# Kernel tuning notes

Hardware: AMD Instinct MI355X
Metric: run time of the kernel (lower is better)

The kernel has to match this reference:

```python
import jax, jax.numpy as jnp
import numpy as np

WH = WW = 8          # window height/width
N_WIN = WH * WW      # tokens per window = 64
DIM = 256
NUM_HEADS = 8
CPB_HIDDEN = 512


def _rel_index():
    # Swin relative position index, shape (N, N), values in [0, (2Wh-1)*(2Ww-1))
    coords = np.stack(np.meshgrid(np.arange(WH), np.arange(WW), indexing='ij'))  # (2,Wh,Ww)
    flat = coords.reshape(2, -1)
    rel = (flat[:, :, None] - flat[:, None, :]).transpose(1, 2, 0)  # (N,N,2)
    rel[..., 0] += WH - 1
    rel[..., 1] += WW - 1
    rel[..., 0] *= 2 * WW - 1
    return rel.sum(-1).astype(np.int32)


def _coords_table():
    # normalized log-spaced continuous relative coordinates, shape (2Wh-1, 2Ww-1, 2)
    h = np.arange(-(WH - 1), WH, dtype=np.float32)
    w = np.arange(-(WW - 1), WW, dtype=np.float32)
    t = np.stack(np.meshgrid(h, w, indexing='ij'), axis=-1)
    t[..., 0] /= WH - 1
    t[..., 1] /= WW - 1
    t *= 8.0
    return (np.sign(t) * np.log2(np.abs(t) + 1.0) / np.log2(8.0)).astype(np.float32)


def setup_inputs() -> dict:
    key = jax.random.key(0)
    ks = jax.random.split(key, 6)
    B_ = 8192  # num_windows * batch
    x = jax.random.normal(ks[0], (B_, N_WIN, DIM), dtype=jnp.float32)
    qkv_weight = jax.random.normal(ks[1], (3 * DIM, DIM), dtype=jnp.float32) * 0.02
    q_bias = jnp.zeros((DIM,), dtype=jnp.float32)
    v_bias = jnp.zeros((DIM,), dtype=jnp.float32)
    logit_scale = jnp.log(10.0) * jnp.ones((NUM_HEADS, 1, 1), dtype=jnp.float32)
    cpb_w1 = jax.random.normal(ks[2], (CPB_HIDDEN, 2), dtype=jnp.float32) * 0.02
    cpb_b1 = jnp.zeros((CPB_HIDDEN,), dtype=jnp.float32)
    cpb_w2 = jax.random.normal(ks[3], (NUM_HEADS, CPB_HIDDEN), dtype=jnp.float32) * 0.02
    proj_w = jax.random.normal(ks[4], (DIM, DIM), dtype=jnp.float32) * 0.02
    proj_b = jnp.zeros((DIM,), dtype=jnp.float32)
    return {
        'x': x, 'qkv_weight': qkv_weight, 'q_bias': q_bias, 'v_bias': v_bias,
        'logit_scale': logit_scale, 'cpb_w1': cpb_w1, 'cpb_b1': cpb_b1,
        'cpb_w2': cpb_w2, 'proj_w': proj_w, 'proj_b': proj_b,
    }


def reference(x, qkv_weight, q_bias, v_bias, logit_scale, cpb_w1, cpb_b1, cpb_w2, proj_w, proj_b):
    B_, N, C = x.shape
    H = NUM_HEADS
    d = C // H
    # qkv projection: k-bias is fixed zero (Swin-V2 convention)
    qkv_b = jnp.concatenate([q_bias, jnp.zeros_like(v_bias), v_bias])
    qkv = x @ qkv_weight.T + qkv_b                       # (B_, N, 3C)
    qkv = qkv.reshape(B_, N, 3, H, d).transpose(2, 0, 3, 1, 4)  # (3, B_, H, N, d)
    q, k, v = qkv[0], qkv[1], qkv[2]
    # cosine attention (F.normalize with eps=1e-12)
    qn = q / jnp.maximum(jnp.linalg.norm(q, axis=-1, keepdims=True), 1e-12)
    kn = k / jnp.maximum(jnp.linalg.norm(k, axis=-1, keepdims=True), 1e-12)
    attn = jnp.einsum('bhnd,bhmd->bhnm', qn, kn)
    scale = jnp.exp(jnp.minimum(logit_scale, jnp.log(100.0)))  # clamp max = log(1/0.01)
    attn = attn * scale                                   # broadcasts (H,1,1)
    # continuous relative position bias via tiny MLP
    table = jnp.asarray(_coords_table())                  # (2Wh-1, 2Ww-1, 2)
    bias_table = jnp.maximum(table @ cpb_w1.T + cpb_b1, 0.0) @ cpb_w2.T  # (.., H)
    bias_table = bias_table.reshape(-1, H)
    idx = jnp.asarray(_rel_index().reshape(-1))
    bias = bias_table[idx].reshape(N, N, H).transpose(2, 0, 1)  # (H, N, N)
    attn = attn + 16.0 * jax.nn.sigmoid(bias)[None]
    attn = jax.nn.softmax(attn, axis=-1)
    out = jnp.einsum('bhnm,bhmd->bhnd', attn, v)          # (B_, H, N, d)
    out = out.transpose(0, 2, 1, 3).reshape(B_, N, C)
    return out @ proj_w.T + proj_b
```

## Files before the change

kernel.cpp:

```cpp
#include <hip/hip_runtime.h>
#include <hip/hip_fp16.h>

typedef _Float16 f16;
typedef _Float16 f16x8 __attribute__((ext_vector_type(8)));
typedef _Float16 f16x4 __attribute__((ext_vector_type(4)));
typedef float f32x4 __attribute__((ext_vector_type(4)));

#define L2E 1.4426950408889634f

#define WQ_OFF   0
#define PW_OFF   393216
#define QB_OFF   524288
#define SC_OFF   527360
#define TBL_OFF  527616
#define BB_OFF   535040


__global__ void prep0(const float* __restrict__ qw, const float* __restrict__ prw,
                      const float* __restrict__ qbias, const float* __restrict__ vbias,
                      const float* __restrict__ ls, char* __restrict__ ws) {
    int t = blockIdx.x * 256 + threadIdx.x;
    f16* wq = (f16*)(ws + WQ_OFF);
    f16* pw = (f16*)(ws + PW_OFF);
    if (t < 196608) wq[t] = (f16)qw[t];
    else            pw[t - 196608] = (f16)prw[t - 196608];
    if (t < 768) {
        float b = t < 256 ? qbias[t] : (t < 512 ? 0.f : vbias[t - 512]);
        ((float*)(ws + QB_OFF))[t] = b;
    }
    if (t < 8) ((float*)(ws + SC_OFF))[t] = expf(fminf(ls[t], 4.6051701859880914f));
}

__device__ __forceinline__ float norm_coord(int u) {
    float v = (float)(u - 7) * (8.0f / 7.0f);
    float s = (v > 0.f) ? 1.f : ((v < 0.f) ? -1.f : 0.f);
    return s * log2f(fabsf(v) + 1.f) * (1.f / 3.f);
}

__global__ void prep1(const float* __restrict__ w1, const float* __restrict__ b1,
                      const float* __restrict__ w2, char* __restrict__ ws) {
    int t = blockIdx.x * 256 + threadIdx.x;
    if (t >= 1800) return;
    int p = t >> 3, h = t & 7;
    float ta = norm_coord(p / 15);
    float tb = norm_coord(p % 15);
    float acc = 0.f;
    for (int j = 0; j < 512; ++j) {
        float hv = fmaf(w1[2 * j], ta, fmaf(w1[2 * j + 1], tb, b1[j]));
        acc = fmaf(fmaxf(hv, 0.f), w2[h * 512 + j], acc);
    }
    ((float*)(ws + TBL_OFF))[p * 8 + h] = acc;
}

__global__ void prep2(char* __restrict__ ws) {
    int t = blockIdx.x * 256 + threadIdx.x;
    int h = t >> 12, i = (t >> 6) & 63, j = t & 63;
    int ri = ((i >> 3) - (j >> 3) + 7) * 15 + ((i & 7) - (j & 7) + 7);
    float bv = ((const float*)(ws + TBL_OFF))[ri * 8 + h];
    float sg = 1.f / (1.f + expf(-bv));
    float sch = ((const float*)(ws + SC_OFF))[h];
    float val = (16.f * sg - sch - 16.f) * L2E + 14.0f;
    int mi = i >> 4, g = (i >> 2) & 3, r = i & 3;
    int nj = j >> 4, c = j & 15;
    int off = h * 4096 + mi * 1024 + nj * 256 + c * 16 + g * 4 + r;
    ((float*)(ws + BB_OFF))[off] = val;
}

#define SWZ(row) (((row) & 7) << 4)
#define LGKM0() asm volatile("s_waitcnt lgkmcnt(0)" ::: "memory")

__global__ __launch_bounds__(512, 2)
void swin_fused(const float* __restrict__ x, const f16* __restrict__ wq,
                const f16* __restrict__ pw, const float* __restrict__ qb,
                const float* __restrict__ sc, const float* __restrict__ bb2,
                const float* __restrict__ pb, float* __restrict__ out) {
    extern __shared__ char lds[];
    const int tid = threadIdx.x;
    const int lane = tid & 63;
    const int w = tid >> 6;
    const int g = lane >> 4;
    const int c = lane & 15;
    const int win = blockIdx.x;
    char* scr = lds + 32768 + w * 5120;

    const float* xw = x + (size_t)win * 16384;
    #pragma unroll
    for (int it = 0; it < 8; ++it) {
        int e4 = tid + it * 512;
        float4 v = ((const float4*)xw)[e4];
        int eidx = e4 * 4;
        int row = eidx >> 8, col = eidx & 255;
        f16x4 h4 = {(f16)v.x, (f16)v.y, (f16)v.z, (f16)v.w};
        int off = ((row << 9) + (col << 1)) ^ SWZ(row);
        *(f16x4*)(lds + off) = h4;
    }
    __syncthreads();

    f16x8 vf[2][2];
    {
        f32x4 acc[2][4] = {};
        for (int kk = 0; kk < 8; ++kk) {
            int kb = kk * 32 + g * 8;
            f16x8 a[4];
            #pragma unroll
            for (int mi = 0; mi < 4; ++mi) {
                int row = mi * 16 + c;
                int off = ((row << 9) + (kb << 1)) ^ SWZ(row);
                a[mi] = *(const f16x8*)(lds + off);
            }
            #pragma unroll
            for (int t = 0; t < 2; ++t) {
                f16x8 b = *(const f16x8*)(wq + (size_t)(512 + w * 32 + t * 16 + c) * 256 + kb);
                #pragma unroll
                for (int mi = 0; mi < 4; ++mi)
                    acc[t][mi] = __builtin_amdgcn_mfma_f32_16x16x32_f16(a[mi], b, acc[t][mi], 0, 0, 0);
            }
        }
        #pragma unroll
        for (int t = 0; t < 2; ++t) {
            float bias = qb[512 + w * 32 + t * 16 + c];
            #pragma unroll
            for (int mi = 0; mi < 4; ++mi) {
                f16x4 h;
                #pragma unroll
                for (int r = 0; r < 4; ++r) h[r] = (f16)(acc[t][mi][r] + bias);
                int off = (t * 16 + c) * 144 + (mi * 16 + g * 4) * 2;
                *(f16x4*)(scr + off) = h;
            }
        }
    }
    LGKM0();
    #pragma unroll
    for (int dt = 0; dt < 2; ++dt)
        #pragma unroll
        for (int kt = 0; kt < 2; ++kt)
            vf[dt][kt] = *(const f16x8*)(scr + (dt * 16 + c) * 144 + kt * 64 + g * 16);
    LGKM0();

    f16x8 qf[4], kf[4];
    {
        f32x4 aq[2][4] = {};
        for (int kk = 0; kk < 8; ++kk) {
            int kb = kk * 32 + g * 8;
            f16x8 a[4];
            #pragma unroll
            for (int mi = 0; mi < 4; ++mi) {
                int row = mi * 16 + c;
                int off = ((row << 9) + (kb << 1)) ^ SWZ(row);
                a[mi] = *(const f16x8*)(lds + off);
            }
            #pragma unroll
            for (int t = 0; t < 2; ++t) {
                f16x8 bq = *(const f16x8*)(wq + (size_t)(w * 32 + t * 16 + c) * 256 + kb);
                #pragma unroll
                for (int mi = 0; mi < 4; ++mi)
                    aq[t][mi] = __builtin_amdgcn_mfma_f32_16x16x32_f16(a[mi], bq, aq[t][mi], 0, 0, 0);
            }
        }
        #pragma unroll
        for (int t = 0; t < 2; ++t) {
            float bias = qb[w * 32 + t * 16 + c];
            #pragma unroll
            for (int mi = 0; mi < 4; ++mi)
                #pragma unroll
                for (int r = 0; r < 4; ++r) aq[t][mi][r] += bias;
        }
        f32x4 rq[4];
        #pragma unroll
        for (int mi = 0; mi < 4; ++mi) {
            #pragma unroll
            for (int r = 0; r < 4; ++r) {
                float pq = aq[0][mi][r] * aq[0][mi][r] + aq[1][mi][r] * aq[1][mi][r];
                pq += __shfl_xor(pq, 1); pq += __shfl_xor(pq, 2);
                pq += __shfl_xor(pq, 4); pq += __shfl_xor(pq, 8);
                rq[mi][r] = __builtin_amdgcn_rsqf(fmaxf(pq, 1e-24f));
            }
        }
        #pragma unroll
        for (int t = 0; t < 2; ++t)
            #pragma unroll
            for (int mi = 0; mi < 4; ++mi)
                #pragma unroll
                for (int r = 0; r < 4; ++r) {
                    int off = (mi * 16 + g * 4 + r) * 80 + (t * 16 + c) * 2;
                    *(f16*)(scr + off) = (f16)(aq[t][mi][r] * rq[mi][r]);
                }
        LGKM0();
        #pragma unroll
        for (int mi = 0; mi < 4; ++mi)
            qf[mi] = *(const f16x8*)(scr + (mi * 16 + c) * 80 + g * 16);
        LGKM0();
    }
    {
        f32x4 ak[2][4] = {};
        for (int kk = 0; kk < 8; ++kk) {
            int kb = kk * 32 + g * 8;
            f16x8 a[4];
            #pragma unroll
            for (int mi = 0; mi < 4; ++mi) {
                int row = mi * 16 + c;
                int off = ((row << 9) + (kb << 1)) ^ SWZ(row);
                a[mi] = *(const f16x8*)(lds + off);
            }
            #pragma unroll
            for (int t = 0; t < 2; ++t) {
                f16x8 bk = *(const f16x8*)(wq + (size_t)(256 + w * 32 + t * 16 + c) * 256 + kb);
                #pragma unroll
                for (int mi = 0; mi < 4; ++mi)
                    ak[t][mi] = __builtin_amdgcn_mfma_f32_16x16x32_f16(a[mi], bk, ak[t][mi], 0, 0, 0);
            }
        }
        f32x4 rk[4];
        #pragma unroll
        for (int mi = 0; mi < 4; ++mi) {
            #pragma unroll
            for (int r = 0; r < 4; ++r) {
                float pk = ak[0][mi][r] * ak[0][mi][r] + ak[1][mi][r] * ak[1][mi][r];
                pk += __shfl_xor(pk, 1); pk += __shfl_xor(pk, 2);
                pk += __shfl_xor(pk, 4); pk += __shfl_xor(pk, 8);
                rk[mi][r] = __builtin_amdgcn_rsqf(fmaxf(pk, 1e-24f));
            }
        }
        #pragma unroll
        for (int t = 0; t < 2; ++t)
            #pragma unroll
            for (int mi = 0; mi < 4; ++mi)
                #pragma unroll
                for (int r = 0; r < 4; ++r) {
                    int off = (mi * 16 + g * 4 + r) * 80 + (t * 16 + c) * 2;
                    *(f16*)(scr + off) = (f16)(ak[t][mi][r] * rk[mi][r]);
                }
        LGKM0();
        #pragma unroll
        for (int nj = 0; nj < 4; ++nj)
            kf[nj] = *(const f16x8*)(scr + (nj * 16 + c) * 80 + g * 16);
        LGKM0();
    }

    const float scl2e = sc[w] * L2E;
    const float* bbw = bb2 + w * 4096;
    f32x4 o[4][2] = {};
    f32x4 rs[4] = {};
    #pragma unroll
    for (int nj = 0; nj < 4; ++nj) {
        #pragma unroll
        for (int mi = 0; mi < 4; ++mi) {
            f32x4 z = {};
            f32x4 s = __builtin_amdgcn_mfma_f32_16x16x32_f16(qf[mi], kf[nj], z, 0, 0, 0);
            f32x4 bb4 = *(const f32x4*)(bbw + mi * 1024 + nj * 256 + c * 16 + g * 4);
            #pragma unroll
            for (int r = 0; r < 4; ++r) {
                float e = exp2f(fmaf(s[r], scl2e, bb4[r]));
                rs[mi][r] += e;
                int off = (mi * 16 + g * 4 + r) * 80 + (((nj & 1) * 16 + c) << 1);
                *(f16*)(scr + off) = (f16)e;
            }
        }
        if (nj == 1 || nj == 3) {
            const int kt = nj >> 1;
            LGKM0();
            f16x8 pa[4];
            #pragma unroll
            for (int mo = 0; mo < 4; ++mo)
                pa[mo] = *(const f16x8*)(scr + (mo * 16 + c) * 80 + g * 16);
            LGKM0();
            #pragma unroll
            for (int mo = 0; mo < 4; ++mo)
                #pragma unroll
                for (int dt = 0; dt < 2; ++dt)
                    o[mo][dt] = __builtin_amdgcn_mfma_f32_16x16x32_f16(pa[mo], vf[dt][kt], o[mo][dt], 0, 0, 0);
        }
    }
    f32x4 rinv[4];
    #pragma unroll
    for (int mi = 0; mi < 4; ++mi)
        #pragma unroll
        for (int r = 0; r < 4; ++r) {
            float t = rs[mi][r];
            t += __shfl_xor(t, 1); t += __shfl_xor(t, 2);
            t += __shfl_xor(t, 4); t += __shfl_xor(t, 8);
            rinv[mi][r] = __builtin_amdgcn_rcpf(t);
        }

    __syncthreads();
    #pragma unroll
    for (int mi = 0; mi < 4; ++mi)
        #pragma unroll
        for (int dt = 0; dt < 2; ++dt)
            #pragma unroll
            for (int r = 0; r < 4; ++r) {
                int row = mi * 16 + g * 4 + r;
                int col = w * 32 + dt * 16 + c;
                int off = ((row << 9) + (col << 1)) ^ SWZ(row);
                *(f16*)(lds + off) = (f16)(o[mi][dt][r] * rinv[mi][r]);
            }
    __syncthreads();

    f32x4 pacc[2][4] = {};
    for (int kk = 0; kk < 8; ++kk) {
        int kb = kk * 32 + g * 8;
        f16x8 a[4];
        #pragma unroll
        for (int mi = 0; mi < 4; ++mi) {
            int row = mi * 16 + c;
            int off = ((row << 9) + (kb << 1)) ^ SWZ(row);
            a[mi] = *(const f16x8*)(lds + off);
        }
        #pragma unroll
        for (int nt = 0; nt < 2; ++nt) {
            f16x8 b = *(const f16x8*)(pw + (size_t)(w * 32 + nt * 16 + c) * 256 + kb);
            #pragma unroll
            for (int mi = 0; mi < 4; ++mi)
                pacc[nt][mi] = __builtin_amdgcn_mfma_f32_16x16x32_f16(a[mi], b, pacc[nt][mi], 0, 0, 0);
        }
    }
    __syncthreads();

    #pragma unroll
    for (int nt = 0; nt < 2; ++nt) {
        float pbias = pb[w * 32 + nt * 16 + c];
        #pragma unroll
        for (int mi = 0; mi < 4; ++mi)
            #pragma unroll
            for (int r = 0; r < 4; ++r) {
                int row = mi * 16 + g * 4 + r;
                int col = w * 32 + nt * 16 + c;
                int off = (row * 1024 + col * 4) ^ ((row & 7) << 4);
                *(float*)(lds + off) = pacc[nt][mi][r] + pbias;
            }
    }
    __syncthreads();
    float4* out4 = (float4*)(out + (size_t)win * 16384);
    #pragma unroll
    for (int it = 0; it < 8; ++it) {
        int e4 = it * 512 + tid;
        int off = (e4 * 16) ^ (((e4 >> 6) & 7) << 4);
        out4[e4] = *(const float4*)(lds + off);
    }
}


extern "C" void kernel_launch(void* const* d_in, const int* in_sizes, int n_in,
                              void* d_out, int out_size, void* d_ws, size_t ws_size,
                              hipStream_t stream) {
    (void)in_sizes; (void)n_in; (void)out_size; (void)ws_size;
    const float* x   = (const float*)d_in[0];
    const float* qw  = (const float*)d_in[1];
    const float* qb_ = (const float*)d_in[2];
    const float* vb_ = (const float*)d_in[3];
    const float* ls  = (const float*)d_in[4];
    const float* w1  = (const float*)d_in[5];
    const float* b1  = (const float*)d_in[6];
    const float* w2  = (const float*)d_in[7];
    const float* prw = (const float*)d_in[8];
    const float* pb  = (const float*)d_in[9];
    float* out = (float*)d_out;
    char* ws = (char*)d_ws;

    prep0<<<1024, 256, 0, stream>>>(qw, prw, qb_, vb_, ls, ws);
    prep1<<<8, 256, 0, stream>>>(w1, b1, w2, ws);
    prep2<<<128, 256, 0, stream>>>(ws);

    (void)hipFuncSetAttribute((const void*)swin_fused,
                              hipFuncAttributeMaxDynamicSharedMemorySize, 73728);
    swin_fused<<<8192, 512, 73728, stream>>>(
        x,
        (const f16*)(ws + WQ_OFF), (const f16*)(ws + PW_OFF),
        (const float*)(ws + QB_OFF), (const float*)(ws + SC_OFF),
        (const float*)(ws + BB_OFF), pb, out);
}
```

Before: 944.6 us.

## Halve block to 4 waves, each wave processing two heads sequentially

The fused window-attention kernel now runs 256 threads per window, with each wave looping over two heads and keeping the first head's output in registers until the shared x tile can be overwritten. Softmax row sums are computed with an extra MFMA against a ones vector instead of shuffle reductions. The output projection writes through LDS in two halves, which reduces dynamic LDS from 72KB to 52KB so more blocks can be resident. In exchange each wave does serial work for two heads and carries more live registers.

```diff
diff --git a/kernel.cpp b/kernel.cpp
--- a/kernel.cpp
+++ b/kernel.cpp
@@ -69,7 +69,7 @@
 #define SWZ(row) (((row) & 7) << 4)
 #define LGKM0() asm volatile("s_waitcnt lgkmcnt(0)" ::: "memory")
 
-__global__ __launch_bounds__(512, 2)
+__global__ __launch_bounds__(256, 2)
 void swin_fused(const float* __restrict__ x, const f16* __restrict__ wq,
                 const f16* __restrict__ pw, const float* __restrict__ qb,
                 const float* __restrict__ sc, const float* __restrict__ bb2,
@@ -85,8 +85,8 @@
 
     const float* xw = x + (size_t)win * 16384;
     #pragma unroll
-    for (int it = 0; it < 8; ++it) {
-        int e4 = tid + it * 512;
+    for (int it = 0; it < 16; ++it) {
+        int e4 = tid + it * 256;
         float4 v = ((const float4*)xw)[e4];
         int eidx = e4 * 4;
         int row = eidx >> 8, col = eidx & 255;
@@ -96,207 +96,246 @@
     }
     __syncthreads();
 
-    f16x8 vf[2][2];
-    {
-        f32x4 acc[2][4] = {};
-        for (int kk = 0; kk < 8; ++kk) {
-            int kb = kk * 32 + g * 8;
-            f16x8 a[4];
+    f16x4 po[4][2];
+
+    for (int hh = 0; hh < 2; ++hh) {
+        const int h = w + hh * 4;
+
+        f16x8 vf[2][2];
+        {
+            f32x4 acc[2][4] = {};
+            #pragma unroll 2
+            for (int kk = 0; kk < 8; ++kk) {
+                int kb = kk * 32 + g * 8;
+                f16x8 a[4];
+                #pragma unroll
+                for (int mi = 0; mi < 4; ++mi) {
+                    int row = mi * 16 + c;
+                    int off = ((row << 9) + (kb << 1)) ^ SWZ(row);
+                    a[mi] = *(const f16x8*)(lds + off);
+                }
+                #pragma unroll
+                for (int t = 0; t < 2; ++t) {
+                    f16x8 b = *(const f16x8*)(wq + (size_t)(512 + h * 32 + t * 16 + c) * 256 + kb);
+                    #pragma unroll
+                    for (int mi = 0; mi < 4; ++mi)
+                        acc[t][mi] = __builtin_amdgcn_mfma_f32_16x16x32_f16(a[mi], b, acc[t][mi], 0, 0, 0);
+                }
+            }
+            #pragma unroll
+            for (int t = 0; t < 2; ++t) {
+                float bias = qb[512 + h * 32 + t * 16 + c];
+                #pragma unroll
+                for (int mi = 0; mi < 4; ++mi) {
+                    f16x4 hv;
+                    #pragma unroll
+                    for (int r = 0; r < 4; ++r) hv[r] = (f16)(acc[t][mi][r] + bias);
+                    int off = (t * 16 + c) * 144 + (mi * 16 + g * 4) * 2;
+                    *(f16x4*)(scr + off) = hv;
+                }
+            }
+        }
+        LGKM0();
+        #pragma unroll
+        for (int dt = 0; dt < 2; ++dt)
+            #pragma unroll
+            for (int kt = 0; kt < 2; ++kt)
+                vf[dt][kt] = *(const f16x8*)(scr + (dt * 16 + c) * 144 + kt * 64 + g * 16);
+        LGKM0();
+
+        f16x8 qf[4], kf[4];
+        {
+            f32x4 aq[2][4] = {};
+            #pragma unroll 2
+            for (int kk = 0; kk < 8; ++kk) {
+                int kb = kk * 32 + g * 8;
+                f16x8 a[4];
+                #pragma unroll
+                for (int mi = 0; mi < 4; ++mi) {
+                    int row = mi * 16 + c;
+                    int off = ((row << 9) + (kb << 1)) ^ SWZ(row);
+                    a[mi] = *(const f16x8*)(lds + off);
+                }
+                #pragma unroll
+                for (int t = 0; t < 2; ++t) {
+                    f16x8 bq = *(const f16x8*)(wq + (size_t)(h * 32 + t * 16 + c) * 256 + kb);
+                    #pragma unroll
+                    for (int mi = 0; mi < 4; ++mi)
+                        aq[t][mi] = __builtin_amdgcn_mfma_f32_16x16x32_f16(a[mi], bq, aq[t][mi], 0, 0, 0);
+                }
+            }
+            #pragma unroll
+            for (int t = 0; t < 2; ++t) {
+                float bias = qb[h * 32 + t * 16 + c];
+                #pragma unroll
+                for (int mi = 0; mi < 4; ++mi)
+                    #pragma unroll
+                    for (int r = 0; r < 4; ++r) aq[t][mi][r] += bias;
+            }
             #pragma unroll
             for (int mi = 0; mi < 4; ++mi) {
-                int row = mi * 16 + c;
-                int off = ((row << 9) + (kb << 1)) ^ SWZ(row);
-                a[mi] = *(const f16x8*)(lds + off);
-            }
-            #pragma unroll
-            for (int t = 0; t < 2; ++t) {
-                f16x8 b = *(const f16x8*)(wq + (size_t)(512 + w * 32 + t * 16 + c) * 256 + kb);
+                #pragma unroll
+                for (int r = 0; r < 4; ++r) {
+                    float pq = aq[0][mi][r] * aq[0][mi][r] + aq[1][mi][r] * aq[1][mi][r];
+                    pq += __shfl_xor(pq, 1); pq += __shfl_xor(pq, 2);
+                    pq += __shfl_xor(pq, 4); pq += __shfl_xor(pq, 8);
+                    float rq = __builtin_amdgcn_rsqf(fmaxf(pq, 1e-24f));
+                    aq[0][mi][r] *= rq; aq[1][mi][r] *= rq;
+                }
+            }
+            #pragma unroll
+            for (int t = 0; t < 2; ++t)
                 #pragma unroll
                 for (int mi = 0; mi < 4; ++mi)
-                    acc[t][mi] = __builtin_amdgcn_mfma_f32_16x16x32_f16(a[mi], b, acc[t][mi], 0, 0, 0);
-            }
-        }
-        #pragma unroll
-        for (int t = 0; t < 2; ++t) {
-            float bias = qb[512 + w * 32 + t * 16 + c];
+                    #pragma unroll
+                    for (int r = 0; r < 4; ++r) {
+                        int off = (mi * 16 + g * 4 + r) * 80 + (t * 16 + c) * 2;
+                        *(f16*)(scr + off) = (f16)aq[t][mi][r];
+                    }
+            LGKM0();
+            #pragma unroll
+            for (int mi = 0; mi < 4; ++mi)
+                qf[mi] = *(const f16x8*)(scr + (mi * 16 + c) * 80 + g * 16);
+            LGKM0();
+        }
+        {
+            f32x4 ak[2][4] = {};
+            #pragma unroll 2
+            for (int kk = 0; kk < 8; ++kk) {
+                int kb = kk * 32 + g * 8;
+                f16x8 a[4];
+                #pragma unroll
+                for (int mi = 0; mi < 4; ++mi) {
+                    int row = mi * 16 + c;
+                    int off = ((row << 9) + (kb << 1)) ^ SWZ(row);
+                    a[mi] = *(const f16x8*)(lds + off);
+                }
+                #pragma unroll
+                for (int t = 0; t < 2; ++t) {
+                    f16x8 bk = *(const f16x8*)(wq + (size_t)(256 + h * 32 + t * 16 + c) * 256 + kb);
+                    #pragma unroll
+                    for (int mi = 0; mi < 4; ++mi)
+                        ak[t][mi] = __builtin_amdgcn_mfma_f32_16x16x32_f16(a[mi], bk, ak[t][mi], 0, 0, 0);
+                }
+            }
             #pragma unroll
             for (int mi = 0; mi < 4; ++mi) {
-                f16x4 h;
-                #pragma unroll
-                for (int r = 0; r < 4; ++r) h[r] = (f16)(acc[t][mi][r] + bias);
-                int off = (t * 16 + c) * 144 + (mi * 16 + g * 4) * 2;
-                *(f16x4*)(scr + off) = h;
-            }
-        }
-    }
-    LGKM0();
+                #pragma unroll
+                for (int r = 0; r < 4; ++r) {
+                    float pk = ak[0][mi][r] * ak[0][mi][r] + ak[1][mi][r] * ak[1][mi][r];
+                    pk += __shfl_xor(pk, 1); pk += __shfl_xor(pk, 2);
+                    pk += __shfl_xor(pk, 4); pk += __shfl_xor(pk, 8);
+                    float rk = __builtin_amdgcn_rsqf(fmaxf(pk, 1e-24f));
+                    ak[0][mi][r] *= rk; ak[1][mi][r] *= rk;
+                }
+            }
+            #pragma unroll
+            for (int t = 0; t < 2; ++t)
+                #pragma unroll
+                for (int mi = 0; mi < 4; ++mi)
+                    #pragma unroll
+                    for (int r = 0; r < 4; ++r) {
+                        int off = (mi * 16 + g * 4 + r) * 80 + (t * 16 + c) * 2;
+                        *(f16*)(scr + off) = (f16)ak[t][mi][r];
+                    }
+            LGKM0();
+            #pragma unroll
+            for (int nj = 0; nj < 4; ++nj)
+                kf[nj] = *(const f16x8*)(scr + (nj * 16 + c) * 80 + g * 16);
+            LGKM0();
+        }
+
+        if (hh == 1) {
+            __syncthreads();
+            const int h0 = w;
+            #pragma unroll
+            for (int mi = 0; mi < 4; ++mi)
+                #pragma unroll
+                for (int dt = 0; dt < 2; ++dt)
+                    #pragma unroll
+                    for (int r = 0; r < 4; ++r) {
+                        int row = mi * 16 + g * 4 + r;
+                        int col = h0 * 32 + dt * 16 + c;
+                        int off = ((row << 9) + (col << 1)) ^ SWZ(row);
+                        *(f16*)(lds + off) = po[mi][dt][r];
+                    }
+        }
+
+        const float scl2e = sc[h] * L2E;
+        const float* bbw = bb2 + h * 4096;
+        f32x4 oo[4][2] = {};
+        f32x4 oaux[4] = {};
+        f16 onev = (c == 0) ? (f16)1.f : (f16)0.f;
+        f16x8 von = {onev, onev, onev, onev, onev, onev, onev, onev};
+        #pragma unroll
+        for (int nj = 0; nj < 4; ++nj) {
+            #pragma unroll
+            for (int mi = 0; mi < 4; ++mi) {
+                f32x4 z = {};
+                f32x4 s = __builtin_amdgcn_mfma_f32_16x16x32_f16(qf[mi], kf[nj], z, 0, 0, 0);
+                f32x4 bb4 = *(const f32x4*)(bbw + mi * 1024 + nj * 256 + c * 16 + g * 4);
+                #pragma unroll
+                for (int r = 0; r < 4; ++r) {
+                    float e = exp2f(fmaf(s[r], scl2e, bb4[r]));
+                    int off = (mi * 16 + g * 4 + r) * 80 + (((nj & 1) * 16 + c) << 1);
+                    *(f16*)(scr + off) = (f16)e;
+                }
+            }
+            if (nj & 1) {
+                const int kt = nj >> 1;
+                LGKM0();
+                f16x8 pa[4];
+                #pragma unroll
+                for (int mo = 0; mo < 4; ++mo)
+                    pa[mo] = *(const f16x8*)(scr + (mo * 16 + c) * 80 + g * 16);
+                LGKM0();
+                #pragma unroll
+                for (int mo = 0; mo < 4; ++mo) {
+                    #pragma unroll
+                    for (int dt = 0; dt < 2; ++dt)
+                        oo[mo][dt] = __builtin_amdgcn_mfma_f32_16x16x32_f16(pa[mo], vf[dt][kt], oo[mo][dt], 0, 0, 0);
+                    oaux[mo] = __builtin_amdgcn_mfma_f32_16x16x32_f16(pa[mo], von, oaux[mo], 0, 0, 0);
+                }
+            }
+        }
+        #pragma unroll
+        for (int mo = 0; mo < 4; ++mo)
+            #pragma unroll
+            for (int r = 0; r < 4; ++r) {
+                float rsum = __shfl(oaux[mo][r], lane & 48);
+                float ri = __builtin_amdgcn_rcpf(rsum);
+                oo[mo][0][r] *= ri;
+                oo[mo][1][r] *= ri;
+            }
+        if (hh == 0) {
+            #pragma unroll
+            for (int mi = 0; mi < 4; ++mi)
+                #pragma unroll
+                for (int dt = 0; dt < 2; ++dt)
+                    #pragma unroll
+                    for (int r = 0; r < 4; ++r)
+                        po[mi][dt][r] = (f16)oo[mi][dt][r];
+        } else {
+            #pragma unroll
+            for (int mi = 0; mi < 4; ++mi)
+                #pragma unroll
+                for (int dt = 0; dt < 2; ++dt)
+                    #pragma unroll
+                    for (int r = 0; r < 4; ++r) {
+                        int row = mi * 16 + g * 4 + r;
+                        int col = h * 32 + dt * 16 + c;
+                        int off = ((row << 9) + (col << 1)) ^ SWZ(row);
+                        *(f16*)(lds + off) = (f16)oo[mi][dt][r];
+                    }
+        }
+    }
+    __syncthreads();
+
+    float pbias[4];
     #pragma unroll
-    for (int dt = 0; dt < 2; ++dt)
-        #pragma unroll
-        for (int kt = 0; kt < 2; ++kt)
-            vf[dt][kt] = *(const f16x8*)(scr + (dt * 16 + c) * 144 + kt * 64 + g * 16);
-    LGKM0();
-
-    f16x8 qf[4], kf[4];
-    {
-        f32x4 aq[2][4] = {};
-        for (int kk = 0; kk < 8; ++kk) {
-            int kb = kk * 32 + g * 8;
-            f16x8 a[4];
-            #pragma unroll
-            for (int mi = 0; mi < 4; ++mi) {
-                int row = mi * 16 + c;
-                int off = ((row << 9) + (kb << 1)) ^ SWZ(row);
-                a[mi] = *(const f16x8*)(lds + off);
-            }
-            #pragma unroll
-            for (int t = 0; t < 2; ++t) {
-                f16x8 bq = *(const f16x8*)(wq + (size_t)(w * 32 + t * 16 + c) * 256 + kb);
-                #pragma unroll
-                for (int mi = 0; mi < 4; ++mi)
-                    aq[t][mi] = __builtin_amdgcn_mfma_f32_16x16x32_f16(a[mi], bq, aq[t][mi], 0, 0, 0);
-            }
-        }
-        #pragma unroll
-        for (int t = 0; t < 2; ++t) {
-            float bias = qb[w * 32 + t * 16 + c];
-            #pragma unroll
-            for (int mi = 0; mi < 4; ++mi)
-                #pragma unroll
-                for (int r = 0; r < 4; ++r) aq[t][mi][r] += bias;
-        }
-        f32x4 rq[4];
-        #pragma unroll
-        for (int mi = 0; mi < 4; ++mi) {
-            #pragma unroll
-            for (int r = 0; r < 4; ++r) {
-                float pq = aq[0][mi][r] * aq[0][mi][r] + aq[1][mi][r] * aq[1][mi][r];
-                pq += __shfl_xor(pq, 1); pq += __shfl_xor(pq, 2);
-                pq += __shfl_xor(pq, 4); pq += __shfl_xor(pq, 8);
-                rq[mi][r] = __builtin_amdgcn_rsqf(fmaxf(pq, 1e-24f));
-            }
-        }
-        #pragma unroll
-        for (int t = 0; t < 2; ++t)
-            #pragma unroll
-            for (int mi = 0; mi < 4; ++mi)
-                #pragma unroll
-                for (int r = 0; r < 4; ++r) {
-                    int off = (mi * 16 + g * 4 + r) * 80 + (t * 16 + c) * 2;
-                    *(f16*)(scr + off) = (f16)(aq[t][mi][r] * rq[mi][r]);
-                }
-        LGKM0();
-        #pragma unroll
-        for (int mi = 0; mi < 4; ++mi)
-            qf[mi] = *(const f16x8*)(scr + (mi * 16 + c) * 80 + g * 16);
-        LGKM0();
-    }
-    {
-        f32x4 ak[2][4] = {};
-        for (int kk = 0; kk < 8; ++kk) {
-            int kb = kk * 32 + g * 8;
-            f16x8 a[4];
-            #pragma unroll
-            for (int mi = 0; mi < 4; ++mi) {
-                int row = mi * 16 + c;
-                int off = ((row << 9) + (kb << 1)) ^ SWZ(row);
-                a[mi] = *(const f16x8*)(lds + off);
-            }
-            #pragma unroll
-            for (int t = 0; t < 2; ++t) {
-                f16x8 bk = *(const f16x8*)(wq + (size_t)(256 + w * 32 + t * 16 + c) * 256 + kb);
-                #pragma unroll
-                for (int mi = 0; mi < 4; ++mi)
-                    ak[t][mi] = __builtin_amdgcn_mfma_f32_16x16x32_f16(a[mi], bk, ak[t][mi], 0, 0, 0);
-            }
-        }
-        f32x4 rk[4];
-        #pragma unroll
-        for (int mi = 0; mi < 4; ++mi) {
-            #pragma unroll
-            for (int r = 0; r < 4; ++r) {
-                float pk = ak[0][mi][r] * ak[0][mi][r] + ak[1][mi][r] * ak[1][mi][r];
-                pk += __shfl_xor(pk, 1); pk += __shfl_xor(pk, 2);
-                pk += __shfl_xor(pk, 4); pk += __shfl_xor(pk, 8);
-                rk[mi][r] = __builtin_amdgcn_rsqf(fmaxf(pk, 1e-24f));
-            }
-        }
-        #pragma unroll
-        for (int t = 0; t < 2; ++t)
-            #pragma unroll
-            for (int mi = 0; mi < 4; ++mi)
-                #pragma unroll
-                for (int r = 0; r < 4; ++r) {
-                    int off = (mi * 16 + g * 4 + r) * 80 + (t * 16 + c) * 2;
-                    *(f16*)(scr + off) = (f16)(ak[t][mi][r] * rk[mi][r]);
-                }
-        LGKM0();
-        #pragma unroll
-        for (int nj = 0; nj < 4; ++nj)
-            kf[nj] = *(const f16x8*)(scr + (nj * 16 + c) * 80 + g * 16);
-        LGKM0();
-    }
-
-    const float scl2e = sc[w] * L2E;
-    const float* bbw = bb2 + w * 4096;
-    f32x4 o[4][2] = {};
-    f32x4 rs[4] = {};
-    #pragma unroll
-    for (int nj = 0; nj < 4; ++nj) {
-        #pragma unroll
-        for (int mi = 0; mi < 4; ++mi) {
-            f32x4 z = {};
-            f32x4 s = __builtin_amdgcn_mfma_f32_16x16x32_f16(qf[mi], kf[nj], z, 0, 0, 0);
-            f32x4 bb4 = *(const f32x4*)(bbw + mi * 1024 + nj * 256 + c * 16 + g * 4);
-            #pragma unroll
-            for (int r = 0; r < 4; ++r) {
-                float e = exp2f(fmaf(s[r], scl2e, bb4[r]));
-                rs[mi][r] += e;
-                int off = (mi * 16 + g * 4 + r) * 80 + (((nj & 1) * 16 + c) << 1);
-                *(f16*)(scr + off) = (f16)e;
-            }
-        }
-        if (nj == 1 || nj == 3) {
-            const int kt = nj >> 1;
-            LGKM0();
-            f16x8 pa[4];
-            #pragma unroll
-            for (int mo = 0; mo < 4; ++mo)
-                pa[mo] = *(const f16x8*)(scr + (mo * 16 + c) * 80 + g * 16);
-            LGKM0();
-            #pragma unroll
-            for (int mo = 0; mo < 4; ++mo)
-                #pragma unroll
-                for (int dt = 0; dt < 2; ++dt)
-                    o[mo][dt] = __builtin_amdgcn_mfma_f32_16x16x32_f16(pa[mo], vf[dt][kt], o[mo][dt], 0, 0, 0);
-        }
-    }
-    f32x4 rinv[4];
-    #pragma unroll
-    for (int mi = 0; mi < 4; ++mi)
-        #pragma unroll
-        for (int r = 0; r < 4; ++r) {
-            float t = rs[mi][r];
-            t += __shfl_xor(t, 1); t += __shfl_xor(t, 2);
-            t += __shfl_xor(t, 4); t += __shfl_xor(t, 8);
-            rinv[mi][r] = __builtin_amdgcn_rcpf(t);
-        }
-
-    __syncthreads();
-    #pragma unroll
-    for (int mi = 0; mi < 4; ++mi)
-        #pragma unroll
-        for (int dt = 0; dt < 2; ++dt)
-            #pragma unroll
-            for (int r = 0; r < 4; ++r) {
-                int row = mi * 16 + g * 4 + r;
-                int col = w * 32 + dt * 16 + c;
-                int off = ((row << 9) + (col << 1)) ^ SWZ(row);
-                *(f16*)(lds + off) = (f16)(o[mi][dt][r] * rinv[mi][r]);
-            }
-    __syncthreads();
-
-    f32x4 pacc[2][4] = {};
+    for (int nt = 0; nt < 4; ++nt) pbias[nt] = pb[w * 64 + nt * 16 + c];
+    f32x4 pacc[4][4] = {};
+    #pragma unroll 2
     for (int kk = 0; kk < 8; ++kk) {
         int kb = kk * 32 + g * 8;
         f16x8 a[4];
@@ -307,8 +346,8 @@
             a[mi] = *(const f16x8*)(lds + off);
         }
         #pragma unroll
-        for (int nt = 0; nt < 2; ++nt) {
-            f16x8 b = *(const f16x8*)(pw + (size_t)(w * 32 + nt * 16 + c) * 256 + kb);
+        for (int nt = 0; nt < 4; ++nt) {
+            f16x8 b = *(const f16x8*)(pw + (size_t)(w * 64 + nt * 16 + c) * 256 + kb);
             #pragma unroll
             for (int mi = 0; mi < 4; ++mi)
                 pacc[nt][mi] = __builtin_amdgcn_mfma_f32_16x16x32_f16(a[mi], b, pacc[nt][mi], 0, 0, 0);
@@ -317,25 +356,29 @@
     __syncthreads();
 
     #pragma unroll
-    for (int nt = 0; nt < 2; ++nt) {
-        float pbias = pb[w * 32 + nt * 16 + c];
-        #pragma unroll
-        for (int mi = 0; mi < 4; ++mi)
-            #pragma unroll
-            for (int r = 0; r < 4; ++r) {
-                int row = mi * 16 + g * 4 + r;
-                int col = w * 32 + nt * 16 + c;
-                int off = (row * 1024 + col * 4) ^ ((row & 7) << 4);
-                *(float*)(lds + off) = pacc[nt][mi][r] + pbias;
-            }
-    }
-    __syncthreads();
-    float4* out4 = (float4*)(out + (size_t)win * 16384);
-    #pragma unroll
-    for (int it = 0; it < 8; ++it) {
-        int e4 = it * 512 + tid;
-        int off = (e4 * 16) ^ (((e4 >> 6) & 7) << 4);
-        out4[e4] = *(const float4*)(lds + off);
+    for (int p = 0; p < 2; ++p) {
+        #pragma unroll
+        for (int nt = 0; nt < 4; ++nt)
+            #pragma unroll
+            for (int m2 = 0; m2 < 2; ++m2) {
+                int mi = p * 2 + m2;
+                #pragma unroll
+                for (int r = 0; r < 4; ++r) {
+                    int row = m2 * 16 + g * 4 + r;
+                    int col = w * 64 + nt * 16 + c;
+                    int off = (row * 1024 + col * 4) ^ ((row & 7) << 4);
+                    *(float*)(lds + off) = pacc[nt][mi][r] + pbias[nt];
+                }
+            }
+        __syncthreads();
+        float4* out4 = (float4*)(out + (size_t)win * 16384 + p * 8192);
+        #pragma unroll
+        for (int it = 0; it < 8; ++it) {
+            int e4 = it * 256 + tid;
+            int off = (e4 * 16) ^ (((e4 >> 6) & 7) << 4);
+            out4[e4] = *(const float4*)(lds + off);
+        }
+        if (p == 0) __syncthreads();
     }
 }
 
@@ -362,8 +405,8 @@
     prep2<<<128, 256, 0, stream>>>(ws);
 
     (void)hipFuncSetAttribute((const void*)swin_fused,
-                              hipFuncAttributeMaxDynamicSharedMemorySize, 73728);
-    swin_fused<<<8192, 512, 73728, stream>>>(
+                              hipFuncAttributeMaxDynamicSharedMemorySize, 53248);
+    swin_fused<<<8192, 256, 53248, stream>>>(
         x,
         (const f16*)(ws + WQ_OFF), (const f16*)(ws + PW_OFF),
         (const float*)(ws + QB_OFF), (const float*)(ws + SC_OFF),
```

New measurement: 772.0 us. -18.3%, faster.
